# Optimization experiments

Measured on AMD Instinct MI355X. Metric: run time of the kernel, lower is better.

Reference implementation:

```python
import jax, jax.numpy as jnp
import numpy as np

D_MODEL = 1024
N_HEADS = 16


def setup_inputs() -> dict:
    key = jax.random.key(0)
    ks = jax.random.split(key, 5)
    B, T, C = 4, 2048, D_MODEL
    x = jax.random.normal(ks[0], (B, T, C), dtype=jnp.float32)
    s = 1.0 / np.sqrt(C)
    W_attn = jax.random.normal(ks[1], (C, 3 * C), dtype=jnp.float32) * s
    b_attn = jnp.zeros((3 * C,), dtype=jnp.float32)
    W_proj = jax.random.normal(ks[2], (C, C), dtype=jnp.float32) * s
    b_proj = jnp.zeros((C,), dtype=jnp.float32)
    return {"x": x, "W_attn": W_attn, "b_attn": b_attn, "W_proj": W_proj, "b_proj": b_proj}


def reference(x, W_attn, b_attn, W_proj, b_proj):
    B, T, C = x.shape
    H = N_HEADS
    hd = C // H
    qkv = x @ W_attn + b_attn                      # [B,T,3C]
    q, k, v = jnp.split(qkv, 3, axis=-1)
    # reshape to [B,H,T,hd]
    q = q.reshape(B, T, H, hd).transpose(0, 2, 1, 3)
    k = k.reshape(B, T, H, hd).transpose(0, 2, 1, 3)
    v = v.reshape(B, T, H, hd).transpose(0, 2, 1, 3)
    scale = 1.0 / jnp.sqrt(jnp.asarray(hd, dtype=x.dtype))
    aff = jnp.einsum('bhqd,bhkd->bhqk', q, k) * scale   # [B,H,T,T]
    causal = jnp.tril(jnp.ones((T, T), dtype=bool))
    aff = jnp.where(causal, aff, jnp.asarray(-jnp.inf, dtype=aff.dtype))
    p = jax.nn.softmax(aff, axis=-1)
    y = jnp.einsum('bhqk,bhkd->bhqd', p, v)             # [B,H,T,hd]
    y = y.transpose(0, 2, 1, 3).reshape(B, T, C)
    return y @ W_proj + b_proj
```

## Files before the change

### kernel.cpp

```cpp
#include <hip/hip_runtime.h>
#include <stdint.h>
#include <math.h>

typedef __attribute__((ext_vector_type(8))) __bf16 bf16x8;
typedef __attribute__((ext_vector_type(4))) __bf16 bf16x4;
typedef __attribute__((ext_vector_type(4))) float f32x4;

#define MFMA16(A, B, C) __builtin_amdgcn_mfma_f32_16x16x32_bf16((A), (B), (C), 0, 0, 0)

#if defined(__has_builtin)
#if __has_builtin(__builtin_amdgcn_exp2f)
#define EXP2(x) __builtin_amdgcn_exp2f(x)
#else
#define EXP2(x) exp2f(x)
#endif
#else
#define EXP2(x) exp2f(x)
#endif

static constexpr int kT  = 2048;
static constexpr int kC  = 1024;
static constexpr int kHD = 64;
#define QSCALE 0.1803368801111204f

__device__ __forceinline__ void g2l16(const void* g, void* l) {
  __builtin_amdgcn_global_load_lds(
      (const __attribute__((address_space(1))) uint32_t*)g,
      (__attribute__((address_space(3))) uint32_t*)l, 16, 0, 0);
}

__global__ __launch_bounds__(256) void k_convert_x(const float* __restrict__ x,
                                                   __bf16* __restrict__ xb) {
  int i = (blockIdx.x * 256 + threadIdx.x) * 4;
  f32x4 v = *(const f32x4*)(x + i);
  bf16x4 o;
  o[0] = (__bf16)v[0]; o[1] = (__bf16)v[1]; o[2] = (__bf16)v[2]; o[3] = (__bf16)v[3];
  *(bf16x4*)(xb + i) = o;
}

__global__ __launch_bounds__(256) void k_transpose_w(const float* __restrict__ src,
                                                     __bf16* __restrict__ dst, int N) {
  __shared__ float t[32][33];
  int k0 = blockIdx.x * 32, n0 = blockIdx.y * 32;
  int c = threadIdx.x & 31, r = threadIdx.x >> 5;
#pragma unroll
  for (int i = 0; i < 4; ++i)
    t[r + i * 8][c] = src[(size_t)(k0 + r + i * 8) * N + n0 + c];
  __syncthreads();
#pragma unroll
  for (int i = 0; i < 4; ++i)
    dst[(size_t)(n0 + r + i * 8) * 1024 + k0 + c] = (__bf16)t[c][r + i * 8];
}

static constexpr int GK = 1024;
static constexpr int GNT = GK / 32;

template <int MODE>
__global__ __launch_bounds__(256, 3) void k_gemm(const __bf16* __restrict__ A,
                                                 const __bf16* __restrict__ Bw,
                                                 const float* __restrict__ bias,
                                                 __bf16* __restrict__ qo,
                                                 __bf16* __restrict__ ko,
                                                 __bf16* __restrict__ vo,
                                                 float* __restrict__ out) {
  __shared__ __bf16 As[3][128 * 32];
  __shared__ __bf16 Bs[3][128 * 32];

  const int tid = threadIdx.x;
  const int wave = tid >> 6, lane = tid & 63;
  const int lo = lane & 15, hi = lane >> 4;
  const int wr = wave & 1, wc = wave >> 1;

  constexpr int NBN = (MODE == 0) ? 24 : 8;
  const int nwg = (int)gridDim.x;
  const int id = (int)blockIdx.x;
  const int wg = (id & 7) * (nwg >> 3) + (id >> 3);
  const int bm = wg / NBN, bn = wg % NBN;
  const int m0 = bm * 128, n0 = bn * 128;

  const int rG0 = tid >> 2, gG0 = (tid & 3) ^ ((rG0 >> 1) & 3);
  const int rG1 = (tid + 256) >> 2, gG1 = ((tid + 256) & 3) ^ ((rG1 >> 1) & 3);
  const __bf16* gaA0 = A + (size_t)(m0 + rG0) * GK + gG0 * 8;
  const __bf16* gaA1 = A + (size_t)(m0 + rG1) * GK + gG1 * 8;
  const __bf16* gbB0 = Bw + (size_t)(n0 + rG0) * GK + gG0 * 8;
  const __bf16* gbB1 = Bw + (size_t)(n0 + rG1) * GK + gG1 * 8;

  const int fsw = (hi ^ ((lo >> 1) & 3)) * 8;
  const int offA = (wr * 64 + lo) * 32 + fsw;
  const int offB = (wc * 64 + lo) * 32 + fsw;

  f32x4 acc[4][4] = {};

#define GSTAGE(jt, bufi)                                  \
  {                                                       \
    g2l16(gaA0 + (jt) * 32, &As[(bufi)][tid * 8]);        \
    g2l16(gaA1 + (jt) * 32, &As[(bufi)][2048 + tid * 8]); \
    g2l16(gbB0 + (jt) * 32, &Bs[(bufi)][tid * 8]);        \
    g2l16(gbB1 + (jt) * 32, &Bs[(bufi)][2048 + tid * 8]); \
  }

  GSTAGE(0, 0);
  GSTAGE(1, 1);
  asm volatile("s_waitcnt vmcnt(4)" ::: "memory");
  __builtin_amdgcn_s_barrier();
  __builtin_amdgcn_sched_barrier(0);

  int rb = 0, rs = 2;
  for (int j = 0; j < GNT; ++j) {
    const __bf16* Ab = &As[rb][0];
    const __bf16* Bb = &Bs[rb][0];
    if (j < GNT - 2) GSTAGE(j + 2, rs);
    bf16x8 af[4], bfr[4];
#pragma unroll
    for (int m = 0; m < 4; ++m) af[m] = *(const bf16x8*)&Ab[offA + m * 512];
#pragma unroll
    for (int n = 0; n < 4; ++n) bfr[n] = *(const bf16x8*)&Bb[offB + n * 512];
    __builtin_amdgcn_s_setprio(1);
#pragma unroll
    for (int m = 0; m < 4; ++m)
#pragma unroll
      for (int n = 0; n < 4; ++n)
        acc[m][n] = MFMA16(af[m], bfr[n], acc[m][n]);
    __builtin_amdgcn_s_setprio(0);
    if (j < GNT - 2) {
      asm volatile("s_waitcnt vmcnt(4)" ::: "memory");
    } else if (j == GNT - 2) {
      asm volatile("s_waitcnt vmcnt(0)" ::: "memory");
    }
    if (j < GNT - 1) {
      __builtin_amdgcn_s_barrier();
      __builtin_amdgcn_sched_barrier(0);
    }
    rb = (rb == 2) ? 0 : rb + 1;
    rs = (rs == 2) ? 0 : rs + 1;
  }
#undef GSTAGE

  if (MODE == 0) {
#pragma unroll
    for (int nj = 0; nj < 4; ++nj) {
      int gn = n0 + wc * 64 + nj * 16 + lo;
      float bv = bias[gn];
      int which = gn >> 10;
      int c = gn & 1023;
      int hh = c >> 6, d = c & 63;
#pragma unroll
      for (int mi = 0; mi < 4; ++mi) {
        int gm = m0 + wr * 64 + mi * 16 + hi * 4;
        int bb = gm >> 11, t0 = gm & 2047;
        if (which == 2) {
          bf16x4 vv;
#pragma unroll
          for (int r = 0; r < 4; ++r) vv[r] = (__bf16)(acc[mi][nj][r] + bv);
          *(bf16x4*)(vo + ((size_t)(bb * 16 + hh) * 64 + d) * 2048 + t0) = vv;
        } else {
#pragma unroll
          for (int r = 0; r < 4; ++r) {
            float val = acc[mi][nj][r] + bv;
            size_t idx = (((size_t)(bb * 16 + hh)) * 2048 + (t0 + r)) * 64 + d;
            if (which == 0)
              qo[idx] = (__bf16)(val * QSCALE);
            else
              ko[idx] = (__bf16)val;
          }
        }
      }
    }
  } else {
#pragma unroll
    for (int nj = 0; nj < 4; ++nj) {
      int gn = n0 + wc * 64 + nj * 16 + lo;
      float bv = bias[gn];
#pragma unroll
      for (int mi = 0; mi < 4; ++mi) {
        int gm = m0 + wr * 64 + mi * 16 + hi * 4;
#pragma unroll
        for (int r = 0; r < 4; ++r)
          out[(size_t)(gm + r) * 1024 + gn] = acc[mi][nj][r] + bv;
      }
    }
  }
}

__global__ __launch_bounds__(256, 4) void k_flash(const __bf16* __restrict__ qb,
                                                  const __bf16* __restrict__ kb,
                                                  const __bf16* __restrict__ vt,
                                                  __bf16* __restrict__ ob) {
  __shared__ __bf16 Ks[2][64 * 64];
  __shared__ __bf16 Vs[2][64 * 64];
  __shared__ __bf16 Ps[4][16 * 64];

  const int id = (int)blockIdx.y * 16 + (int)blockIdx.x;
  const int xcd = id & 7, jj = id >> 3;
  const int bh = (jj & 7) * 8 + xcd;
  const int xs = jj >> 3;
  const int b = bh >> 4, h = bh & 15;
  const int tid = threadIdx.x, wave = tid >> 6, lane = tid & 63;
  const int lo = lane & 15, hi = lane >> 4;

  const int qrow[2] = { (31 - xs) * 64 + wave * 16, xs * 64 + wave * 16 };

  bf16x8 qf[2][2];
#pragma unroll
  for (int rg = 0; rg < 2; ++rg) {
    const __bf16* Qp = qb + ((size_t)bh * kT + qrow[rg]) * kHD;
    qf[rg][0] = *(const bf16x8*)(Qp + lo * kHD + hi * 8);
    qf[rg][1] = *(const bf16x8*)(Qp + lo * kHD + 32 + hi * 8);
  }

  bf16x8 onesf;
#pragma unroll
  for (int e = 0; e < 8; ++e) onesf[e] = (lo == 0) ? (__bf16)1.0f : (__bf16)0.0f;

  f32x4 acc[2][4] = {};
  f32x4 accsum[2] = {};

  const __bf16* Kbase = kb + (size_t)bh * kT * kHD;
  const __bf16* Vbase = vt + (size_t)bh * kHD * kT;

  int srcK[2], srcV[2];
#pragma unroll
  for (int p = 0; p < 2; ++p) {
    int g = wave * 64 + lane + p * 256;
    int r = g >> 3, c = g & 7;
    int cs = c ^ (r & 7);
    srcK[p] = r * kHD + cs * 8;
    srcV[p] = r * kT + cs * 8;
  }
  const int sw0 = (hi ^ (lo & 7)) * 8;
  const int sw1 = ((hi + 4) ^ (lo & 7)) * 8;
  const int psw0 = (hi ^ (lo >> 1)) * 8;
  const int psw1 = ((hi + 4) ^ (lo >> 1)) * 8;

  const int nt = 32 - xs;

#pragma unroll
  for (int p = 0; p < 2; ++p) {
    g2l16(Kbase + srcK[p], &Ks[0][wave * 512 + p * 2048]);
    g2l16(Vbase + srcV[p], &Vs[0][wave * 512 + p * 2048]);
  }

  for (int it = 0; it < nt; ++it) {
    const int kt = it * 64;
    const int pb = it & 1;
    const bool both = (it <= xs);

    __syncthreads();

    if (it + 1 < nt) {
      const int kn = kt + 64;
#pragma unroll
      for (int p = 0; p < 2; ++p) {
        g2l16(Kbase + kn * kHD + srcK[p], &Ks[1 - pb][wave * 512 + p * 2048]);
        g2l16(Vbase + kn + srcV[p],       &Vs[1 - pb][wave * 512 + p * 2048]);
      }
    }

    const __bf16* Kt = &Ks[pb][0];
    const __bf16* Vt = &Vs[pb][0];
    f32x4 s[2][4];
    __builtin_amdgcn_s_setprio(1);
#pragma unroll
    for (int j = 0; j < 4; ++j) {
      const int row = (j * 16 + lo) * 64;
      bf16x8 kf0 = *(const bf16x8*)&Kt[row + sw0];
      bf16x8 kf1 = *(const bf16x8*)&Kt[row + sw1];
      f32x4 z = {};
      z = MFMA16(qf[0][0], kf0, z);
      z = MFMA16(qf[0][1], kf1, z);
      s[0][j] = z;
      if (both) {
        f32x4 z1 = {};
        z1 = MFMA16(qf[1][0], kf0, z1);
        z1 = MFMA16(qf[1][1], kf1, z1);
        s[1][j] = z1;
      }
    }
    __builtin_amdgcn_s_setprio(0);

    bf16x8 pf[2][2];
#pragma unroll
    for (int rg = 0; rg < 2; ++rg) {
      if (rg == 1 && !both) break;
      const int q0 = qrow[rg] + hi * 4;
      if (kt + 63 > q0) {
#pragma unroll
        for (int j = 0; j < 4; ++j)
#pragma unroll
          for (int r = 0; r < 4; ++r)
            if (kt + j * 16 + lo > q0 + r) s[rg][j][r] = -INFINITY;
      }
#pragma unroll
      for (int j = 0; j < 4; ++j)
#pragma unroll
        for (int r = 0; r < 4; ++r)
          s[rg][j][r] = EXP2(s[rg][j][r]);
      __bf16* Pw = &Ps[wave][0];
#pragma unroll
      for (int j = 0; j < 4; ++j)
#pragma unroll
        for (int r = 0; r < 4; ++r) {
          const int q = hi * 4 + r;
          Pw[q * 64 + (((j * 2 + (lo >> 3)) ^ (q >> 1)) * 8) + (lo & 7)] =
              (__bf16)s[rg][j][r];
        }
      pf[rg][0] = *(const bf16x8*)&Pw[lo * 64 + psw0];
      pf[rg][1] = *(const bf16x8*)&Pw[lo * 64 + psw1];
    }

    __builtin_amdgcn_s_setprio(1);
    accsum[0] = MFMA16(pf[0][0], onesf, accsum[0]);
    accsum[0] = MFMA16(pf[0][1], onesf, accsum[0]);
    if (both) {
      accsum[1] = MFMA16(pf[1][0], onesf, accsum[1]);
      accsum[1] = MFMA16(pf[1][1], onesf, accsum[1]);
    }
#pragma unroll
    for (int jd = 0; jd < 4; ++jd) {
      const int row = (jd * 16 + lo) * 64;
      bf16x8 vf0 = *(const bf16x8*)&Vt[row + sw0];
      bf16x8 vf1 = *(const bf16x8*)&Vt[row + sw1];
      acc[0][jd] = MFMA16(pf[0][0], vf0, acc[0][jd]);
      acc[0][jd] = MFMA16(pf[0][1], vf1, acc[0][jd]);
      if (both) {
        acc[1][jd] = MFMA16(pf[1][0], vf0, acc[1][jd]);
        acc[1][jd] = MFMA16(pf[1][1], vf1, acc[1][jd]);
      }
    }
    __builtin_amdgcn_s_setprio(0);
  }

#pragma unroll
  for (int rg = 0; rg < 2; ++rg) {
    float inv[4];
#pragma unroll
    for (int r = 0; r < 4; ++r)
      inv[r] = 1.0f / __shfl(accsum[rg][r], hi * 16, 64);
    __bf16* Op = ob + ((size_t)b * kT + qrow[rg]) * kC + h * kHD;
#pragma unroll
    for (int jd = 0; jd < 4; ++jd)
#pragma unroll
      for (int r = 0; r < 4; ++r)
        Op[(hi * 4 + r) * kC + jd * 16 + lo] = (__bf16)(acc[rg][jd][r] * inv[r]);
  }
}

extern "C" void kernel_launch(void* const* d_in, const int* in_sizes, int n_in,
                              void* d_out, int out_size, void* d_ws, size_t ws_size,
                              hipStream_t stream) {
  const float* x      = (const float*)d_in[0];
  const float* W_attn = (const float*)d_in[1];
  const float* b_attn = (const float*)d_in[2];
  const float* W_proj = (const float*)d_in[3];
  const float* b_proj = (const float*)d_in[4];
  float* out = (float*)d_out;

  char* ws = (char*)d_ws;
  __bf16* xb  = (__bf16*)(ws + 0);
  __bf16* ob  = (__bf16*)(ws + 0);
  __bf16* wab = (__bf16*)(ws + 16777216);
  __bf16* wpb = (__bf16*)(ws + 23068672);
  __bf16* qbf = (__bf16*)(ws + 25165824);
  __bf16* kbf = (__bf16*)(ws + 41943040);
  __bf16* vtb = (__bf16*)(ws + 58720256);

  k_convert_x<<<8192, 256, 0, stream>>>(x, xb);
  k_transpose_w<<<dim3(32, 96), 256, 0, stream>>>(W_attn, wab, 3072);
  k_transpose_w<<<dim3(32, 32), 256, 0, stream>>>(W_proj, wpb, 1024);
  k_gemm<0><<<dim3(1536), 256, 0, stream>>>(xb, wab, b_attn, qbf, kbf, vtb, nullptr);
  k_flash<<<dim3(16, 64), 256, 0, stream>>>(qbf, kbf, vtb, ob);
  k_gemm<1><<<dim3(512), 256, 0, stream>>>(ob, wpb, b_proj, nullptr, nullptr, nullptr, out);
}
```

Baseline: 261.5 us.

## Rewrite flash attention with 32x32 MFMA, register-resident P and 128-row tiles

The attention kernel moves from 16x16x32 MFMA to 32x32x16 MFMA and computes S transposed, so the P fragment comes straight out of the S accumulator in registers. This removes the per-wave LDS round trip for P and the ones-vector MFMA used for row sums, which are now a register reduction plus a cross-half shuffle. Each block handles 128-query tiles (paired causal halves), so the grid drops to 512 blocks with lower occupancy (launch bounds 2). The V-transpose write in the QKV GEMM gets an XOR permutation on the token index to match the new fragment ordering.

```diff
diff --git a/kernel.cpp b/kernel.cpp
--- a/kernel.cpp
+++ b/kernel.cpp
@@ -5,8 +5,10 @@
 typedef __attribute__((ext_vector_type(8))) __bf16 bf16x8;
 typedef __attribute__((ext_vector_type(4))) __bf16 bf16x4;
 typedef __attribute__((ext_vector_type(4))) float f32x4;
+typedef __attribute__((ext_vector_type(16))) float f32x16;
 
 #define MFMA16(A, B, C) __builtin_amdgcn_mfma_f32_16x16x32_bf16((A), (B), (C), 0, 0, 0)
+#define MFMA32(A, B, C) __builtin_amdgcn_mfma_f32_32x32x16_bf16((A), (B), (C), 0, 0, 0)
 
 #if defined(__has_builtin)
 #if __has_builtin(__builtin_amdgcn_exp2f)
@@ -149,10 +151,11 @@
         int gm = m0 + wr * 64 + mi * 16 + hi * 4;
         int bb = gm >> 11, t0 = gm & 2047;
         if (which == 2) {
+          int t0p = t0 ^ ((((t0 >> 2) ^ (t0 >> 3)) & 1) * 12);
           bf16x4 vv;
 #pragma unroll
           for (int r = 0; r < 4; ++r) vv[r] = (__bf16)(acc[mi][nj][r] + bv);
-          *(bf16x4*)(vo + ((size_t)(bb * 16 + hh) * 64 + d) * 2048 + t0) = vv;
+          *(bf16x4*)(vo + ((size_t)(bb * 16 + hh) * 64 + d) * 2048 + t0p) = vv;
         } else {
 #pragma unroll
           for (int r = 0; r < 4; ++r) {
@@ -182,38 +185,35 @@
   }
 }
 
-__global__ __launch_bounds__(256, 4) void k_flash(const __bf16* __restrict__ qb,
+__global__ __launch_bounds__(256, 2) void k_flash(const __bf16* __restrict__ qb,
                                                   const __bf16* __restrict__ kb,
                                                   const __bf16* __restrict__ vt,
                                                   __bf16* __restrict__ ob) {
   __shared__ __bf16 Ks[2][64 * 64];
   __shared__ __bf16 Vs[2][64 * 64];
-  __shared__ __bf16 Ps[4][16 * 64];
-
-  const int id = (int)blockIdx.y * 16 + (int)blockIdx.x;
+
+  const int id = (int)blockIdx.x;
   const int xcd = id & 7, jj = id >> 3;
   const int bh = (jj & 7) * 8 + xcd;
   const int xs = jj >> 3;
   const int b = bh >> 4, h = bh & 15;
   const int tid = threadIdx.x, wave = tid >> 6, lane = tid & 63;
-  const int lo = lane & 15, hi = lane >> 4;
-
-  const int qrow[2] = { (31 - xs) * 64 + wave * 16, xs * 64 + wave * 16 };
-
-  bf16x8 qf[2][2];
+  const int l31 = lane & 31, hi32 = lane >> 5;
+  const int gx = l31 & 7;
+
+  const int qrow[2] = { (15 - xs) * 128 + wave * 32, xs * 128 + wave * 32 };
+
+  bf16x8 qf[2][4];
 #pragma unroll
   for (int rg = 0; rg < 2; ++rg) {
-    const __bf16* Qp = qb + ((size_t)bh * kT + qrow[rg]) * kHD;
-    qf[rg][0] = *(const bf16x8*)(Qp + lo * kHD + hi * 8);
-    qf[rg][1] = *(const bf16x8*)(Qp + lo * kHD + 32 + hi * 8);
-  }
-
-  bf16x8 onesf;
-#pragma unroll
-  for (int e = 0; e < 8; ++e) onesf[e] = (lo == 0) ? (__bf16)1.0f : (__bf16)0.0f;
-
-  f32x4 acc[2][4] = {};
-  f32x4 accsum[2] = {};
+    const __bf16* Qp = qb + ((size_t)bh * kT + qrow[rg] + l31) * kHD + hi32 * 8;
+#pragma unroll
+    for (int ks = 0; ks < 4; ++ks)
+      qf[rg][ks] = *(const bf16x8*)(Qp + ks * 16);
+  }
+
+  f32x16 acc[2][2] = {};
+  float srow[2] = {0.0f, 0.0f};
 
   const __bf16* Kbase = kb + (size_t)bh * kT * kHD;
   const __bf16* Vbase = vt + (size_t)bh * kHD * kT;
@@ -227,12 +227,8 @@
     srcK[p] = r * kHD + cs * 8;
     srcV[p] = r * kT + cs * 8;
   }
-  const int sw0 = (hi ^ (lo & 7)) * 8;
-  const int sw1 = ((hi + 4) ^ (lo & 7)) * 8;
-  const int psw0 = (hi ^ (lo >> 1)) * 8;
-  const int psw1 = ((hi + 4) ^ (lo >> 1)) * 8;
-
-  const int nt = 32 - xs;
+
+  const int nt = 32 - 2 * xs;
 
 #pragma unroll
   for (int p = 0; p < 2; ++p) {
@@ -243,7 +239,7 @@
   for (int it = 0; it < nt; ++it) {
     const int kt = it * 64;
     const int pb = it & 1;
-    const bool both = (it <= xs);
+    const bool both = (it <= 2 * xs + 1);
 
     __syncthreads();
 
@@ -258,90 +254,73 @@
 
     const __bf16* Kt = &Ks[pb][0];
     const __bf16* Vt = &Vs[pb][0];
-    f32x4 s[2][4];
+
+    bf16x8 pa[2][4];
+
+#pragma unroll
+    for (int kb2 = 0; kb2 < 2; ++kb2) {
+      bf16x8 ka[4];
+#pragma unroll
+      for (int ks = 0; ks < 4; ++ks)
+        ka[ks] = *(const bf16x8*)&Kt[(kb2 * 32 + l31) * 64 +
+                                     (((ks * 2 + hi32) ^ gx) * 8)];
+#pragma unroll
+      for (int rg = 0; rg < 2; ++rg) {
+        if (rg == 1 && !both) break;
+        f32x16 s = {};
+        __builtin_amdgcn_s_setprio(1);
+#pragma unroll
+        for (int ks = 0; ks < 4; ++ks) s = MFMA32(ka[ks], qf[rg][ks], s);
+        __builtin_amdgcn_s_setprio(0);
+        const int qg = qrow[rg] + l31;
+        const int kbs = kt + kb2 * 32 + 4 * hi32;
+        if (kt + kb2 * 32 + 31 > qrow[rg]) {
+#pragma unroll
+          for (int i = 0; i < 16; ++i)
+            if (kbs + (i & 3) + 8 * (i >> 2) > qg) s[i] = -INFINITY;
+        }
+#pragma unroll
+        for (int i = 0; i < 16; ++i) s[i] = EXP2(s[i]);
+        float sm = 0.0f;
+#pragma unroll
+        for (int i = 0; i < 16; ++i) sm += s[i];
+        srow[rg] += sm;
+#pragma unroll
+        for (int a = 0; a < 2; ++a) {
+          bf16x8 p;
+#pragma unroll
+          for (int e = 0; e < 8; ++e) p[e] = (__bf16)s[8 * a + e];
+          pa[rg][kb2 * 2 + a] = p;
+        }
+      }
+    }
+
     __builtin_amdgcn_s_setprio(1);
 #pragma unroll
-    for (int j = 0; j < 4; ++j) {
-      const int row = (j * 16 + lo) * 64;
-      bf16x8 kf0 = *(const bf16x8*)&Kt[row + sw0];
-      bf16x8 kf1 = *(const bf16x8*)&Kt[row + sw1];
-      f32x4 z = {};
-      z = MFMA16(qf[0][0], kf0, z);
-      z = MFMA16(qf[0][1], kf1, z);
-      s[0][j] = z;
-      if (both) {
-        f32x4 z1 = {};
-        z1 = MFMA16(qf[1][0], kf0, z1);
-        z1 = MFMA16(qf[1][1], kf1, z1);
-        s[1][j] = z1;
+    for (int db = 0; db < 2; ++db) {
+#pragma unroll
+      for (int ks = 0; ks < 4; ++ks) {
+        bf16x8 vb = *(const bf16x8*)&Vt[(db * 32 + l31) * 64 +
+                                        (((ks * 2 + hi32) ^ gx) * 8)];
+        acc[0][db] = MFMA32(pa[0][ks], vb, acc[0][db]);
+        if (both) acc[1][db] = MFMA32(pa[1][ks], vb, acc[1][db]);
       }
     }
     __builtin_amdgcn_s_setprio(0);
-
-    bf16x8 pf[2][2];
-#pragma unroll
-    for (int rg = 0; rg < 2; ++rg) {
-      if (rg == 1 && !both) break;
-      const int q0 = qrow[rg] + hi * 4;
-      if (kt + 63 > q0) {
-#pragma unroll
-        for (int j = 0; j < 4; ++j)
-#pragma unroll
-          for (int r = 0; r < 4; ++r)
-            if (kt + j * 16 + lo > q0 + r) s[rg][j][r] = -INFINITY;
-      }
-#pragma unroll
-      for (int j = 0; j < 4; ++j)
-#pragma unroll
-        for (int r = 0; r < 4; ++r)
-          s[rg][j][r] = EXP2(s[rg][j][r]);
-      __bf16* Pw = &Ps[wave][0];
-#pragma unroll
-      for (int j = 0; j < 4; ++j)
-#pragma unroll
-        for (int r = 0; r < 4; ++r) {
-          const int q = hi * 4 + r;
-          Pw[q * 64 + (((j * 2 + (lo >> 3)) ^ (q >> 1)) * 8) + (lo & 7)] =
-              (__bf16)s[rg][j][r];
-        }
-      pf[rg][0] = *(const bf16x8*)&Pw[lo * 64 + psw0];
-      pf[rg][1] = *(const bf16x8*)&Pw[lo * 64 + psw1];
-    }
-
-    __builtin_amdgcn_s_setprio(1);
-    accsum[0] = MFMA16(pf[0][0], onesf, accsum[0]);
-    accsum[0] = MFMA16(pf[0][1], onesf, accsum[0]);
-    if (both) {
-      accsum[1] = MFMA16(pf[1][0], onesf, accsum[1]);
-      accsum[1] = MFMA16(pf[1][1], onesf, accsum[1]);
-    }
-#pragma unroll
-    for (int jd = 0; jd < 4; ++jd) {
-      const int row = (jd * 16 + lo) * 64;
-      bf16x8 vf0 = *(const bf16x8*)&Vt[row + sw0];
-      bf16x8 vf1 = *(const bf16x8*)&Vt[row + sw1];
-      acc[0][jd] = MFMA16(pf[0][0], vf0, acc[0][jd]);
-      acc[0][jd] = MFMA16(pf[0][1], vf1, acc[0][jd]);
-      if (both) {
-        acc[1][jd] = MFMA16(pf[1][0], vf0, acc[1][jd]);
-        acc[1][jd] = MFMA16(pf[1][1], vf1, acc[1][jd]);
-      }
-    }
-    __builtin_amdgcn_s_setprio(0);
   }
 
 #pragma unroll
   for (int rg = 0; rg < 2; ++rg) {
-    float inv[4];
-#pragma unroll
-    for (int r = 0; r < 4; ++r)
-      inv[r] = 1.0f / __shfl(accsum[rg][r], hi * 16, 64);
+    float tot = srow[rg] + __shfl_xor(srow[rg], 32, 64);
+    float invt = 1.0f / tot;
     __bf16* Op = ob + ((size_t)b * kT + qrow[rg]) * kC + h * kHD;
 #pragma unroll
-    for (int jd = 0; jd < 4; ++jd)
-#pragma unroll
-      for (int r = 0; r < 4; ++r)
-        Op[(hi * 4 + r) * kC + jd * 16 + lo] = (__bf16)(acc[rg][jd][r] * inv[r]);
+    for (int i = 0; i < 16; ++i) {
+      int q = (i & 3) + 8 * (i >> 2) + 4 * hi32;
+      float inv = __shfl(invt, q, 64);
+      Op[(size_t)q * kC + l31]      = (__bf16)(acc[rg][0][i] * inv);
+      Op[(size_t)q * kC + 32 + l31] = (__bf16)(acc[rg][1][i] * inv);
+    }
   }
 }
 
@@ -368,6 +347,6 @@
   k_transpose_w<<<dim3(32, 96), 256, 0, stream>>>(W_attn, wab, 3072);
   k_transpose_w<<<dim3(32, 32), 256, 0, stream>>>(W_proj, wpb, 1024);
   k_gemm<0><<<dim3(1536), 256, 0, stream>>>(xb, wab, b_attn, qbf, kbf, vtb, nullptr);
-  k_flash<<<dim3(16, 64), 256, 0, stream>>>(qbf, kbf, vtb, ob);
+  k_flash<<<dim3(512), 256, 0, stream>>>(qbf, kbf, vtb, ob);
   k_gemm<1><<<dim3(512), 256, 0, stream>>>(ob, wpb, b_proj, nullptr, nullptr, nullptr, out);
 }
```

Measured after the change: 241.9 us. 1.08x faster.
